# Performance work log

Measured on AMD Instinct MI355X. Metric: run time of the kernel, lower is better.

The kernel has to match this reference:

```python
import jax, jax.numpy as jnp
import numpy as np

B, NUM_PEAKS, PEAK_SIZE = 2, 64, 1000
MOTIF, HID, DEPTH, PROF_K = 640, 256, 7, 75


def conv1d(x, w, b, dilation=1):
    # x: (N, C, L), w: (O, I, K), valid padding
    out = jax.lax.conv_general_dilated(
        x, w, window_strides=(1,), padding='VALID',
        rhs_dilation=(dilation,), dimension_numbers=('NCH', 'OIH', 'NCH'))
    return out + b[None, :, None]


def setup_inputs() -> dict:
    key = jax.random.key(0)
    ks = jax.random.split(key, 10)
    L = NUM_PEAKS * PEAK_SIZE
    x = jax.random.normal(ks[0], (B, L, MOTIF), dtype=jnp.float32)
    peak_split = jnp.full((B * NUM_PEAKS,), PEAK_SIZE, dtype=jnp.int64) if jax.config.jax_enable_x64 else jnp.full((B * NUM_PEAKS,), PEAK_SIZE, dtype=jnp.int32)
    n_peaks = jnp.full((B,), NUM_PEAKS, dtype=jnp.int32)
    # parameters (kaiming-ish small init)
    w_proj = jax.random.normal(ks[1], (HID, MOTIF, 1), dtype=jnp.float32) / np.sqrt(MOTIF)
    b_proj = jnp.zeros((HID,), jnp.float32)
    w_dil = jax.random.normal(ks[2], (DEPTH, HID, HID, 3), dtype=jnp.float32) / np.sqrt(3 * HID)
    b_dil = jnp.zeros((DEPTH, HID), jnp.float32)
    w_prof = jax.random.normal(ks[3], (1, HID, PROF_K), dtype=jnp.float32) / np.sqrt(PROF_K * HID)
    b_prof = jnp.zeros((1,), jnp.float32)
    w_atpm = jax.random.normal(ks[4], (1, HID), dtype=jnp.float32) / np.sqrt(HID)
    b_atpm = jnp.zeros((1,), jnp.float32)
    return {
        'x': x, 'peak_split': peak_split, 'n_peaks': n_peaks, 'max_n_peaks': NUM_PEAKS,
        'w_proj': w_proj, 'b_proj': b_proj, 'w_dil': w_dil, 'b_dil': b_dil,
        'w_prof': w_prof, 'b_prof': b_prof, 'w_atpm': w_atpm, 'b_atpm': b_atpm,
    }


def reference(x, peak_split, n_peaks, max_n_peaks,
              w_proj, b_proj, w_dil, b_dil, w_prof, b_prof, w_atpm, b_atpm):
    # fast path: all samples have max_n_peaks uniform-size peaks
    batch, length, _ = x.shape
    num_peaks = int(np.asarray(n_peaks)[0])
    peak_size = length // num_peaks
    # 1x1 motif projection: (B, L, MOTIF) -> (B, HID, L)
    h = conv1d(jnp.transpose(x, (0, 2, 1)), w_proj, b_proj)
    # split into peaks: (B*num_peaks, HID, peak_size)
    h = jnp.transpose(h, (0, 2, 1)).reshape(batch * num_peaks, peak_size, HID)
    h = jnp.transpose(h, (0, 2, 1))
    # dilated conv tower with residual crop
    for i in range(DEPTH):
        dilation = 2 ** (i + 1)
        out = conv1d(h, w_dil[i], b_dil[i], dilation=dilation)
        crop = (h.shape[-1] - out.shape[-1]) // 2
        h = jax.nn.relu(out) + h[..., crop:-crop]
    peak_atpm = h.mean(axis=2)                      # (N, HID)
    peak_profile = conv1d(h, w_prof, b_prof)        # (N, 1, out_len)
    peak_atpm = jax.nn.softplus(peak_atpm @ w_atpm.T + b_atpm)
    peak_atpm = peak_atpm.reshape(batch, num_peaks, 1)
    peak_profile = jax.nn.softplus(peak_profile.reshape(batch, -1))
    return (peak_atpm, peak_profile)
```

## Files before the change

kernel.cpp:

```cpp
#include <hip/hip_runtime.h>
#include <hip/hip_bf16.h>
#include <math.h>

#define HID 256
#define MOTIF 640
#define PEAK 1000
#define NPEAKS 128
#define DEPTHN 7
#define PROFK 75
#define FINLEN 492
#define PROFLEN 418

typedef unsigned short u16;
typedef unsigned int u32;
typedef _Float16 f16x8 __attribute__((ext_vector_type(8)));
typedef float f32x16 __attribute__((ext_vector_type(16)));

__device__ __forceinline__ u16 f2h(float f) {
    _Float16 h = (_Float16)f; u16 b; __builtin_memcpy(&b, &h, 2); return b;
}
__device__ __forceinline__ float h2f(u16 b) {
    _Float16 h; __builtin_memcpy(&h, &b, 2); return (float)h;
}
__device__ __forceinline__ float hlo(u32 u) { return h2f((u16)(u & 0xffff)); }
__device__ __forceinline__ float hhi(u32 u) { return h2f((u16)(u >> 16)); }
__device__ __forceinline__ u32 pk2h(float a, float b) {
    return (u32)f2h(a) | ((u32)f2h(b) << 16);
}

__device__ __forceinline__ void gll16(const void* g, void* l) {
    __builtin_amdgcn_global_load_lds(
        (const __attribute__((address_space(1))) void*)g,
        (__attribute__((address_space(3))) void*)l, 16, 0, 0);
}

__global__ __launch_bounds__(256) void conv_wdil_all(const float* __restrict__ w,
                                                     u16* __restrict__ wf,
                                                     float* __restrict__ zp) {
    const int layer = blockIdx.y;
    int i = blockIdx.x * 256 + threadIdx.x;
    if (layer == 0 && i < NPEAKS) zp[i] = 0.f;
    const float* wl = w + (size_t)layer * HID * HID * 3;
    u16* wfl = wf + (size_t)layer * (3 * HID * HID);
    int cil = i & 15; int j = i >> 4;
    int c = j & 255; j >>= 8;
    int ci16 = j & 15; int k = j >> 4;
    wfl[i] = f2h(wl[((size_t)c * HID + ci16 * 16 + cil) * 3 + k]);
}

__global__ __launch_bounds__(256) void conv_wproj(const float* __restrict__ w,
                                                  u16* __restrict__ wf) {
    int i = blockIdx.x * 256 + threadIdx.x;
    if (i >= MOTIF * HID) return;
    int ml = i & 15;
    int c = (i >> 4) & 255;
    int m16 = i >> 12;
    wf[i] = f2h(w[(size_t)c * MOTIF + m16 * 16 + ml]);
}

template<int TAPS, int KCI, int DIL, bool SRCF32, bool RESID, bool ATPM>
__global__ __launch_bounds__(256, 3) void mfma_gemm(
    const void* __restrict__ src, int in_len, int in_stride,
    const u16* __restrict__ wf, const float* __restrict__ bias,
    u16* __restrict__ dst, int out_len,
    const float* __restrict__ watpm, float* part)
{
    constexpr int R = 128 + (TAPS - 1) * DIL;
    __shared__ __attribute__((aligned(16))) u16 Bs[R * 64];
    __shared__ float aw[4];
    const int tid = threadIdx.x;
    const int wave = tid >> 6, lane = tid & 63;
    const int col = lane & 31, half = lane >> 5;
    const int cg = wave & 1, tg = wave >> 1;
    const int t0 = blockIdx.x * 128;
    const int c0 = blockIdx.y * 128;
    const int n  = blockIdx.z;

    const float* snf = (const float*)src + (size_t)n * in_len * in_stride;
    const u16*   snh = (const u16*)src + (size_t)n * in_len * in_stride;

    f32x16 acc[2][2];
    #pragma unroll
    for (int cs = 0; cs < 2; ++cs)
        #pragma unroll
        for (int ts = 0; ts < 2; ++ts)
            #pragma unroll
            for (int q = 0; q < 16; ++q) acc[cs][ts][q] = 0.f;

    for (int ci0 = 0; ci0 < KCI; ci0 += 64) {
        __syncthreads();
        if (SRCF32) {
            for (int s = tid; s < R * 8; s += 256) {
                const int r = s >> 3, ch = s & 7;
                int g = t0 + r; if (g > in_len - 1) g = in_len - 1;
                u16* d = &Bs[(size_t)(((r << 3) + (ch ^ (r & 7))) << 3)];
                const float* p = snf + (size_t)g * in_stride + ci0 + ch * 8;
                float4 a = *(const float4*)p;
                float4 b = *(const float4*)(p + 4);
                uint4 o;
                o.x = pk2h(a.x, a.y); o.y = pk2h(a.z, a.w);
                o.z = pk2h(b.x, b.y); o.w = pk2h(b.z, b.w);
                *(uint4*)d = o;
            }
        } else {
            constexpr int ITERS = (R * 8 + 255) / 256;
            #pragma unroll
            for (int it = 0; it < ITERS; ++it) {
                const int s = it * 256 + tid;
                if (s < R * 8) {
                    const int r = s >> 3, ch = s & 7;
                    int g = t0 + r; if (g > in_len - 1) g = in_len - 1;
                    const u16* gp = snh + (size_t)g * in_stride + ci0 + ((ch ^ (r & 7)) << 3);
                    u16* lp = Bs + ((size_t)s << 3);
                    gll16(gp, lp);
                }
            }
            asm volatile("s_waitcnt vmcnt(0)" ::: "memory");
        }
        __syncthreads();
        #pragma unroll
        for (int k = 0; k < TAPS; ++k) {
            #pragma unroll
            for (int s2 = 0; s2 < 4; ++s2) {
                const int ktile = k * (KCI / 16) + (ci0 >> 4) + s2;
                f16x8 bfv[2];
                #pragma unroll
                for (int ts = 0; ts < 2; ++ts) {
                    const int row = tg * 64 + ts * 32 + col + k * DIL;
                    const int slot = (s2 * 2 + half) ^ (row & 7);
                    bfv[ts] = *reinterpret_cast<const f16x8*>(
                        &Bs[(size_t)(((row << 3) + slot) << 3)]);
                }
                #pragma unroll
                for (int cs = 0; cs < 2; ++cs) {
                    const f16x8 af = *reinterpret_cast<const f16x8*>(
                        wf + ((size_t)(ktile * 256 + c0 + cg * 64 + cs * 32 + col) * 16 + half * 8));
                    acc[cs][0] = __builtin_amdgcn_mfma_f32_32x32x16_f16(af, bfv[0], acc[cs][0], 0, 0, 0);
                    acc[cs][1] = __builtin_amdgcn_mfma_f32_32x32x16_f16(af, bfv[1], acc[cs][1], 0, 0, 0);
                }
            }
        }
    }

    float apart = 0.f;
    #pragma unroll
    for (int ts = 0; ts < 2; ++ts) {
        const int t = t0 + tg * 64 + ts * 32 + col;
        if (t >= out_len) continue;
        const float* resf = snf + (size_t)(t + DIL) * in_stride;
        const u16*   resh = snh + (size_t)(t + DIL) * in_stride;
        u16* oh = dst + ((size_t)n * out_len + t) * HID;
        #pragma unroll
        for (int cs = 0; cs < 2; ++cs) {
            #pragma unroll
            for (int g = 0; g < 4; ++g) {
                const int c = c0 + cg * 64 + cs * 32 + g * 8 + half * 4;
                float4 bv = *(const float4*)(bias + c);
                float v0 = acc[cs][ts][g * 4 + 0] + bv.x;
                float v1 = acc[cs][ts][g * 4 + 1] + bv.y;
                float v2 = acc[cs][ts][g * 4 + 2] + bv.z;
                float v3 = acc[cs][ts][g * 4 + 3] + bv.w;
                if (RESID) {
                    if (SRCF32) {
                        float4 r = *(const float4*)(resf + c);
                        v0 = fmaxf(v0, 0.f) + r.x;
                        v1 = fmaxf(v1, 0.f) + r.y;
                        v2 = fmaxf(v2, 0.f) + r.z;
                        v3 = fmaxf(v3, 0.f) + r.w;
                    } else {
                        uint2 r = *(const uint2*)(resh + c);
                        v0 = fmaxf(v0, 0.f) + hlo(r.x);
                        v1 = fmaxf(v1, 0.f) + hhi(r.x);
                        v2 = fmaxf(v2, 0.f) + hlo(r.y);
                        v3 = fmaxf(v3, 0.f) + hhi(r.y);
                    }
                }
                if (ATPM) {
                    float4 wv = *(const float4*)(watpm + c);
                    apart += v0 * wv.x + v1 * wv.y + v2 * wv.z + v3 * wv.w;
                }
                uint2 o; o.x = pk2h(v0, v1); o.y = pk2h(v2, v3);
                *(uint2*)(oh + c) = o;
            }
        }
    }
    if (ATPM) {
        #pragma unroll
        for (int off = 32; off; off >>= 1) apart += __shfl_down(apart, off, 64);
        if (lane == 0) aw[wave] = apart;
        __syncthreads();
        if (tid == 0) atomicAdd(part + n, aw[0] + aw[1] + aw[2] + aw[3]);
    }
}

__global__ void atpm_fin(const float* __restrict__ part,
                         const float* __restrict__ batpm, float* __restrict__ out) {
    int i = threadIdx.x;
    float tot = part[i] / (float)FINLEN + batpm[0];
    out[i] = fmaxf(tot, 0.f) + log1pf(expf(-fabsf(tot)));
}

__global__ __launch_bounds__(256) void prof_kernel(
    const u16* __restrict__ h, const float* __restrict__ wprof,
    const float* __restrict__ bprof, float* __restrict__ out)
{
    __shared__ __attribute__((aligned(16))) float hs[64 * 204];
    __shared__ float red[128 * 8];
    const int tid = threadIdx.x;
    const int wave = tid >> 6, lane = tid & 63;
    const int ts = lane & 31, hw = lane >> 5;
    const int cig = wave * 2 + hw;
    const int n = blockIdx.y, t0 = blockIdx.x * 128;
    const u16* hn = h + (size_t)n * FINLEN * HID;
    float acc[4] = {0.f, 0.f, 0.f, 0.f};

    for (int ci0 = 0; ci0 < HID; ci0 += 64) {
        __syncthreads();
        {
            const int ci = tid & 63, rg = tid >> 6;
            for (int base = 0; base < 204; base += 16) {
                const int r0 = base + rg * 4;
                if (r0 >= 204) continue;
                float4 v;
                float* vp = (float*)&v;
                #pragma unroll
                for (int j = 0; j < 4; ++j) {
                    int g = t0 + r0 + j; if (g > FINLEN - 1) g = FINLEN - 1;
                    vp[j] = h2f(hn[(size_t)g * HID + ci0 + ci]);
                }
                *(float4*)&hs[ci * 204 + r0] = v;
            }
        }
        __syncthreads();
        for (int ci = 0; ci < 8; ++ci) {
            const int cia = cig * 8 + ci;
            const float4* hrow = (const float4*)&hs[cia * 204];
            const float* wrow = wprof + (size_t)(ci0 + cia) * PROFK;
            float wqf[84];
            #pragma unroll
            for (int q = 0; q < 3; ++q) wqf[q] = 0.f;
            #pragma unroll
            for (int q = 78; q < 84; ++q) wqf[q] = 0.f;
            #pragma unroll
            for (int k = 0; k < PROFK; ++k) wqf[k + 3] = wrow[k];
            #pragma unroll
            for (int m = 0; m < 20; ++m) {
                float4 h4 = hrow[ts + m];
                const float* hp = (const float*)&h4;
                #pragma unroll
                for (int j = 0; j < 4; ++j) {
                    #pragma unroll
                    for (int a = 0; a < 4; ++a) {
                        acc[a] += wqf[4 * m + j - a + 3] * hp[j];
                    }
                }
            }
        }
    }
    #pragma unroll
    for (int a = 0; a < 4; ++a) red[(ts * 4 + a) * 8 + cig] = acc[a];
    __syncthreads();
    if (tid < 128) {
        float s = 0.f;
        #pragma unroll
        for (int c8 = 0; c8 < 8; ++c8) s += red[tid * 8 + c8];
        const int t = t0 + tid;
        if (t < PROFLEN) {
            float v = s + bprof[0];
            out[(size_t)n * PROFLEN + t] = fmaxf(v, 0.f) + log1pf(expf(-fabsf(v)));
        }
    }
}

extern "C" void kernel_launch(void* const* d_in, const int* in_sizes, int n_in,
                              void* d_out, int out_size, void* d_ws, size_t ws_size,
                              hipStream_t stream) {
    const float* x     = (const float*)d_in[0];
    const float* wproj = (const float*)d_in[4];
    const float* bproj = (const float*)d_in[5];
    const float* wdil  = (const float*)d_in[6];
    const float* bdil  = (const float*)d_in[7];
    const float* wprof = (const float*)d_in[8];
    const float* bprof = (const float*)d_in[9];
    const float* watpm = (const float*)d_in[10];
    const float* batpm = (const float*)d_in[11];
    float* outAtpm = (float*)d_out;
    float* outProf = outAtpm + NPEAKS;

    char* ws = (char*)d_ws;
    u16* hA    = (u16*)ws;
    u16* hB    = (u16*)(ws + 65536000);
    u16* wpf   = (u16*)(ws + 131072000);
    u16* wslot = (u16*)(ws + 131399680);
    float* part = (float*)(ws + 134152192);

    conv_wproj<<<(MOTIF * HID + 255) / 256, 256, 0, stream>>>(wproj, wpf);
    conv_wdil_all<<<dim3(768, DEPTHN), 256, 0, stream>>>(wdil, wslot, part);

    mfma_gemm<1, MOTIF, 0, true, false, false><<<dim3(8, 2, NPEAKS), 256, 0, stream>>>(
        x, PEAK, MOTIF, wpf, bproj, hA, PEAK, nullptr, nullptr);

    #define LAYER(i, DIL, SRC, DST, INL, OUTL, TT)                                           \
        mfma_gemm<3, HID, DIL, false, true, false><<<dim3(TT, 2, NPEAKS), 256, 0, stream>>>( \
            SRC, INL, HID, wslot + (size_t)(i) * (3 * HID * HID),                            \
            bdil + (size_t)(i) * HID, DST, OUTL, nullptr, nullptr);
    LAYER(0,   2, hA, hB, 1000, 996, 8)
    LAYER(1,   4, hB, hA,  996, 988, 8)
    LAYER(2,   8, hA, hB,  988, 972, 8)
    LAYER(3,  16, hB, hA,  972, 940, 8)
    LAYER(4,  32, hA, hB,  940, 876, 7)
    LAYER(5,  64, hB, hA,  876, 748, 6)
    #undef LAYER
    mfma_gemm<3, HID, 128, false, true, true><<<dim3(4, 2, NPEAKS), 256, 0, stream>>>(
        hA, 748, HID, wslot + (size_t)6 * (3 * HID * HID), bdil + (size_t)6 * HID,
        hB, 492, watpm, part);

    atpm_fin<<<1, 128, 0, stream>>>(part, batpm, outAtpm);
    prof_kernel<<<dim3(4, NPEAKS), 256, 0, stream>>>(hB, wprof, bprof, outProf);
}
```

Baseline: 1.299 ms.

## Load MFMA B operands directly from global memory instead of LDS staging

```diff
diff --git a/kernel.cpp b/kernel.cpp
--- a/kernel.cpp
+++ b/kernel.cpp
@@ -27,11 +27,13 @@
 __device__ __forceinline__ u32 pk2h(float a, float b) {
     return (u32)f2h(a) | ((u32)f2h(b) << 16);
 }
-
-__device__ __forceinline__ void gll16(const void* g, void* l) {
-    __builtin_amdgcn_global_load_lds(
-        (const __attribute__((address_space(1))) void*)g,
-        (__attribute__((address_space(3))) void*)l, 16, 0, 0);
+__device__ __forceinline__ f16x8 cvt8(float4 a, float4 b) {
+    f16x8 r;
+    r[0] = (_Float16)a.x; r[1] = (_Float16)a.y;
+    r[2] = (_Float16)a.z; r[3] = (_Float16)a.w;
+    r[4] = (_Float16)b.x; r[5] = (_Float16)b.y;
+    r[6] = (_Float16)b.z; r[7] = (_Float16)b.w;
+    return r;
 }
 
 __global__ __launch_bounds__(256) void conv_wdil_all(const float* __restrict__ w,
@@ -65,8 +67,6 @@
     u16* __restrict__ dst, int out_len,
     const float* __restrict__ watpm, float* part)
 {
-    constexpr int R = 128 + (TAPS - 1) * DIL;
-    __shared__ __attribute__((aligned(16))) u16 Bs[R * 64];
     __shared__ float aw[4];
     const int tid = threadIdx.x;
     const int wave = tid >> 6, lane = tid & 63;
@@ -87,57 +87,36 @@
             #pragma unroll
             for (int q = 0; q < 16; ++q) acc[cs][ts][q] = 0.f;
 
-    for (int ci0 = 0; ci0 < KCI; ci0 += 64) {
-        __syncthreads();
-        if (SRCF32) {
-            for (int s = tid; s < R * 8; s += 256) {
-                const int r = s >> 3, ch = s & 7;
-                int g = t0 + r; if (g > in_len - 1) g = in_len - 1;
-                u16* d = &Bs[(size_t)(((r << 3) + (ch ^ (r & 7))) << 3)];
-                const float* p = snf + (size_t)g * in_stride + ci0 + ch * 8;
-                float4 a = *(const float4*)p;
-                float4 b = *(const float4*)(p + 4);
-                uint4 o;
-                o.x = pk2h(a.x, a.y); o.y = pk2h(a.z, a.w);
-                o.z = pk2h(b.x, b.y); o.w = pk2h(b.z, b.w);
-                *(uint4*)d = o;
-            }
-        } else {
-            constexpr int ITERS = (R * 8 + 255) / 256;
-            #pragma unroll
-            for (int it = 0; it < ITERS; ++it) {
-                const int s = it * 256 + tid;
-                if (s < R * 8) {
-                    const int r = s >> 3, ch = s & 7;
-                    int g = t0 + r; if (g > in_len - 1) g = in_len - 1;
-                    const u16* gp = snh + (size_t)g * in_stride + ci0 + ((ch ^ (r & 7)) << 3);
-                    u16* lp = Bs + ((size_t)s << 3);
-                    gll16(gp, lp);
-                }
-            }
-            asm volatile("s_waitcnt vmcnt(0)" ::: "memory");
-        }
-        __syncthreads();
-        #pragma unroll
-        for (int k = 0; k < TAPS; ++k) {
-            #pragma unroll
-            for (int s2 = 0; s2 < 4; ++s2) {
-                const int ktile = k * (KCI / 16) + (ci0 >> 4) + s2;
-                f16x8 bfv[2];
-                #pragma unroll
-                for (int ts = 0; ts < 2; ++ts) {
-                    const int row = tg * 64 + ts * 32 + col + k * DIL;
-                    const int slot = (s2 * 2 + half) ^ (row & 7);
-                    bfv[ts] = *reinterpret_cast<const f16x8*>(
-                        &Bs[(size_t)(((row << 3) + slot) << 3)]);
-                }
-                #pragma unroll
-                for (int cs = 0; cs < 2; ++cs) {
-                    const f16x8 af = *reinterpret_cast<const f16x8*>(
-                        wf + ((size_t)(ktile * 256 + c0 + cg * 64 + cs * 32 + col) * 16 + half * 8));
-                    acc[cs][0] = __builtin_amdgcn_mfma_f32_32x32x16_f16(af, bfv[0], acc[cs][0], 0, 0, 0);
-                    acc[cs][1] = __builtin_amdgcn_mfma_f32_32x32x16_f16(af, bfv[1], acc[cs][1], 0, 0, 0);
-                }
+    int trc[2];
+    {
+        const int tb = t0 + tg * 64 + col;
+        trc[0] = tb      < out_len ? tb      : out_len - 1;
+        trc[1] = tb + 32 < out_len ? tb + 32 : out_len - 1;
+    }
+    const u16* wfp = wf + (size_t)(c0 + cg * 64 + col) * 16 + half * 8;
+
+    #pragma unroll
+    for (int k = 0; k < TAPS; ++k) {
+        size_t bb0 = (size_t)(trc[0] + k * DIL) * in_stride + half * 8;
+        size_t bb1 = (size_t)(trc[1] + k * DIL) * in_stride + half * 8;
+        #pragma unroll
+        for (int kt = 0; kt < KCI / 16; ++kt) {
+            const int ktile = k * (KCI / 16) + kt;
+            f16x8 bfv[2];
+            if (SRCF32) {
+                const float4* p0 = (const float4*)(snf + bb0 + kt * 16);
+                const float4* p1 = (const float4*)(snf + bb1 + kt * 16);
+                bfv[0] = cvt8(p0[0], p0[1]);
+                bfv[1] = cvt8(p1[0], p1[1]);
+            } else {
+                bfv[0] = *(const f16x8*)(snh + bb0 + kt * 16);
+                bfv[1] = *(const f16x8*)(snh + bb1 + kt * 16);
+            }
+            #pragma unroll
+            for (int cs = 0; cs < 2; ++cs) {
+                const f16x8 af = *(const f16x8*)(wfp + ((size_t)ktile * 256 + cs * 32) * 16);
+                acc[cs][0] = __builtin_amdgcn_mfma_f32_32x32x16_f16(af, bfv[0], acc[cs][0], 0, 0, 0);
+                acc[cs][1] = __builtin_amdgcn_mfma_f32_32x32x16_f16(af, bfv[1], acc[cs][1], 0, 0, 0);
             }
         }
     }
```

New measurement: 1.639 ms. 26.2% more time.

## Double-buffer weight and activation tiles in LDS with async prefetch pipeline

Applied to the files above, without the earlier changes.

```diff
diff --git a/kernel.cpp b/kernel.cpp
--- a/kernel.cpp
+++ b/kernel.cpp
@@ -58,15 +58,26 @@
     wf[i] = f2h(w[(size_t)c * MOTIF + m16 * 16 + ml]);
 }
 
-template<int TAPS, int KCI, int DIL, bool SRCF32, bool RESID, bool ATPM>
+template<int TAPS, int KCI, int CCI, int DIL, bool SRCF32, bool RESID, bool ATPM>
 __global__ __launch_bounds__(256, 3) void mfma_gemm(
     const void* __restrict__ src, int in_len, int in_stride,
     const u16* __restrict__ wf, const float* __restrict__ bias,
     u16* __restrict__ dst, int out_len,
     const float* __restrict__ watpm, float* part)
 {
-    constexpr int R = 128 + (TAPS - 1) * DIL;
-    __shared__ __attribute__((aligned(16))) u16 Bs[R * 64];
+    constexpr int R    = 128 + (TAPS - 1) * DIL;
+    constexpr int GR   = CCI / 8;
+    constexpr int SUBS = CCI / 16;
+    constexpr int KTC  = TAPS * SUBS;
+    constexpr int NC   = KCI / CCI;
+    constexpr int ASLOTS = KTC * 256;
+    constexpr int AIT  = KTC;
+    constexpr int BSLOTS = R * GR;
+    constexpr int BIT  = (BSLOTS + 255) / 256;
+    constexpr int NIF  = SRCF32 ? AIT : (AIT + BIT);
+
+    __shared__ __attribute__((aligned(16))) u16 As[2][ASLOTS * 8];
+    __shared__ __attribute__((aligned(16))) u16 Bs[2][(BSLOTS + 64) * 8];
     __shared__ float aw[4];
     const int tid = threadIdx.x;
     const int wave = tid >> 6, lane = tid & 63;
@@ -87,58 +98,83 @@
             #pragma unroll
             for (int q = 0; q < 16; ++q) acc[cs][ts][q] = 0.f;
 
-    for (int ci0 = 0; ci0 < KCI; ci0 += 64) {
-        __syncthreads();
-        if (SRCF32) {
-            for (int s = tid; s < R * 8; s += 256) {
-                const int r = s >> 3, ch = s & 7;
-                int g = t0 + r; if (g > in_len - 1) g = in_len - 1;
-                u16* d = &Bs[(size_t)(((r << 3) + (ch ^ (r & 7))) << 3)];
-                const float* p = snf + (size_t)g * in_stride + ci0 + ch * 8;
+    auto stageA = [&](int cc, int b) {
+        const int kt0 = (cc * CCI) >> 4;
+        #pragma unroll
+        for (int it = 0; it < AIT; ++it) {
+            const int s = it * 256 + tid;
+            const int ktl = s >> 8;
+            const int c = (s & 255) >> 1, hf = s & 1;
+            const int k = ktl / SUBS, sub = ktl % SUBS;
+            const int ktg = k * (KCI / 16) + kt0 + sub;
+            gll16(wf + (size_t)(ktg * 256 + c0 + c) * 16 + hf * 8,
+                  &As[b][(size_t)s * 8]);
+        }
+    };
+    auto stageB = [&](int cc, int b) {
+        const int ci0 = cc * CCI;
+        #pragma unroll
+        for (int it = 0; it < BIT; ++it) {
+            int s = it * 256 + tid;
+            if (s >= BSLOTS) s = BSLOTS - 1;
+            const int r = s / GR, ch = s % GR;
+            int g = t0 + r; if (g > in_len - 1) g = in_len - 1;
+            const int chs = ch ^ (r & (GR - 1));
+            if (SRCF32) {
+                const float* p = snf + (size_t)g * in_stride + ci0 + chs * 8;
                 float4 a = *(const float4*)p;
-                float4 b = *(const float4*)(p + 4);
+                float4 bq = *(const float4*)(p + 4);
                 uint4 o;
                 o.x = pk2h(a.x, a.y); o.y = pk2h(a.z, a.w);
-                o.z = pk2h(b.x, b.y); o.w = pk2h(b.z, b.w);
-                *(uint4*)d = o;
-            }
-        } else {
-            constexpr int ITERS = (R * 8 + 255) / 256;
-            #pragma unroll
-            for (int it = 0; it < ITERS; ++it) {
-                const int s = it * 256 + tid;
-                if (s < R * 8) {
-                    const int r = s >> 3, ch = s & 7;
-                    int g = t0 + r; if (g > in_len - 1) g = in_len - 1;
-                    const u16* gp = snh + (size_t)g * in_stride + ci0 + ((ch ^ (r & 7)) << 3);
-                    u16* lp = Bs + ((size_t)s << 3);
-                    gll16(gp, lp);
-                }
-            }
-            asm volatile("s_waitcnt vmcnt(0)" ::: "memory");
-        }
-        __syncthreads();
+                o.z = pk2h(bq.x, bq.y); o.w = pk2h(bq.z, bq.w);
+                *(uint4*)&Bs[b][(size_t)s * 8] = o;
+            } else {
+                gll16(snh + (size_t)g * in_stride + ci0 + chs * 8,
+                      &Bs[b][(size_t)s * 8]);
+            }
+        }
+    };
+    auto compute = [&](int b) {
         #pragma unroll
         for (int k = 0; k < TAPS; ++k) {
             #pragma unroll
-            for (int s2 = 0; s2 < 4; ++s2) {
-                const int ktile = k * (KCI / 16) + (ci0 >> 4) + s2;
-                f16x8 bfv[2];
+            for (int sub = 0; sub < SUBS; ++sub) {
+                const int ktl = k * SUBS + sub;
+                f16x8 bf[2];
                 #pragma unroll
                 for (int ts = 0; ts < 2; ++ts) {
                     const int row = tg * 64 + ts * 32 + col + k * DIL;
-                    const int slot = (s2 * 2 + half) ^ (row & 7);
-                    bfv[ts] = *reinterpret_cast<const f16x8*>(
-                        &Bs[(size_t)(((row << 3) + slot) << 3)]);
+                    const int sl = row * GR + ((sub * 2 + half) ^ (row & (GR - 1)));
+                    bf[ts] = *reinterpret_cast<const f16x8*>(&Bs[b][(size_t)sl * 8]);
                 }
                 #pragma unroll
                 for (int cs = 0; cs < 2; ++cs) {
                     const f16x8 af = *reinterpret_cast<const f16x8*>(
-                        wf + ((size_t)(ktile * 256 + c0 + cg * 64 + cs * 32 + col) * 16 + half * 8));
-                    acc[cs][0] = __builtin_amdgcn_mfma_f32_32x32x16_f16(af, bfv[0], acc[cs][0], 0, 0, 0);
-                    acc[cs][1] = __builtin_amdgcn_mfma_f32_32x32x16_f16(af, bfv[1], acc[cs][1], 0, 0, 0);
-                }
-            }
+                        &As[b][(size_t)(ktl * 256 + (cg * 64 + cs * 32 + col) * 2 + half) * 8]);
+                    acc[cs][0] = __builtin_amdgcn_mfma_f32_32x32x16_f16(af, bf[0], acc[cs][0], 0, 0, 0);
+                    acc[cs][1] = __builtin_amdgcn_mfma_f32_32x32x16_f16(af, bf[1], acc[cs][1], 0, 0, 0);
+                }
+            }
+        }
+    };
+
+    if (SRCF32) { stageB(0, 0); stageA(0, 0); stageB(1, 1); stageA(1, 1); }
+    else        { stageA(0, 0); stageB(0, 0); stageA(1, 1); stageB(1, 1); }
+
+    #pragma unroll
+    for (int c = 0; c < NC; ++c) {
+        if (SRCF32) asm volatile("s_waitcnt lgkmcnt(0)" ::: "memory");
+        if (c + 1 < NC) asm volatile("s_waitcnt vmcnt(%0)" :: "i"(NIF) : "memory");
+        else            asm volatile("s_waitcnt vmcnt(0)" ::: "memory");
+        __builtin_amdgcn_s_barrier();
+        asm volatile("" ::: "memory");
+        compute(c & 1);
+        asm volatile("" ::: "memory");
+        __builtin_amdgcn_s_barrier();
+        asm volatile("" ::: "memory");
+        if (c + 2 < NC) {
+            if (SRCF32) { stageB(c + 2, c & 1); stageA(c + 2, c & 1); }
+            else        { stageA(c + 2, c & 1); stageB(c + 2, c & 1); }
         }
     }
 
@@ -297,12 +333,12 @@
     conv_wproj<<<(MOTIF * HID + 255) / 256, 256, 0, stream>>>(wproj, wpf);
     conv_wdil_all<<<dim3(768, DEPTHN), 256, 0, stream>>>(wdil, wslot, part);
 
-    mfma_gemm<1, MOTIF, 0, true, false, false><<<dim3(8, 2, NPEAKS), 256, 0, stream>>>(
+    mfma_gemm<1, MOTIF, 32, 0, true, false, false><<<dim3(8, 2, NPEAKS), 256, 0, stream>>>(
         x, PEAK, MOTIF, wpf, bproj, hA, PEAK, nullptr, nullptr);
 
-    #define LAYER(i, DIL, SRC, DST, INL, OUTL, TT)                                           \
-        mfma_gemm<3, HID, DIL, false, true, false><<<dim3(TT, 2, NPEAKS), 256, 0, stream>>>( \
-            SRC, INL, HID, wslot + (size_t)(i) * (3 * HID * HID),                            \
+    #define LAYER(i, DIL, SRC, DST, INL, OUTL, TT)                                              \
+        mfma_gemm<3, HID, 16, DIL, false, true, false><<<dim3(TT, 2, NPEAKS), 256, 0, stream>>>( \
+            SRC, INL, HID, wslot + (size_t)(i) * (3 * HID * HID),                               \
             bdil + (size_t)(i) * HID, DST, OUTL, nullptr, nullptr);
     LAYER(0,   2, hA, hB, 1000, 996, 8)
     LAYER(1,   4, hB, hA,  996, 988, 8)
@@ -311,7 +347,7 @@
     LAYER(4,  32, hA, hB,  940, 876, 7)
     LAYER(5,  64, hB, hA,  876, 748, 6)
     #undef LAYER
-    mfma_gemm<3, HID, 128, false, true, true><<<dim3(4, 2, NPEAKS), 256, 0, stream>>>(
+    mfma_gemm<3, HID, 16, 128, false, true, true><<<dim3(4, 2, NPEAKS), 256, 0, stream>>>(
         hA, 748, HID, wslot + (size_t)6 * (3 * HID * HID), bdil + (size_t)6 * HID,
         hB, 492, watpm, part);
 
```

New measurement: 1.155 ms. 11.0% less time.
